# Kernel tuning notes

Measured on AMD Instinct MI355X. Metric: run time of the kernel, lower is better.

The kernel has to match this reference:

```python
import jax, jax.numpy as jnp
import numpy as np

NUM_HEADS = 16


def spike(x):
    # forward of SpikeFunction: Heaviside step
    return (x > 0).astype(x.dtype)


def setup_inputs() -> dict:
    key = jax.random.key(0)
    ks = jax.random.split(key, 11)
    B, S, D = 2, 2048, 1024
    s = 1.0 / np.sqrt(D)
    return {
        "query": jax.random.normal(ks[0], (B, S, D), jnp.float32),
        "key": jax.random.normal(ks[1], (B, S, D), jnp.float32),
        "value": jax.random.normal(ks[2], (B, S, D), jnp.float32),
        "Wq": jax.random.normal(ks[3], (D, D), jnp.float32) * s,
        "bq": jnp.zeros((D,), jnp.float32),
        "Wk": jax.random.normal(ks[4], (D, D), jnp.float32) * s,
        "bk": jnp.zeros((D,), jnp.float32),
        "Wv": jax.random.normal(ks[5], (D, D), jnp.float32) * s,
        "bv": jnp.zeros((D,), jnp.float32),
        "Wo": jax.random.normal(ks[6], (D, D), jnp.float32) * s,
        "bo": jnp.zeros((D,), jnp.float32),
    }


def reference(query, key, value, Wq, bq, Wk, bk, Wv, bv, Wo, bo):
    B, S, D = query.shape
    H = NUM_HEADS
    hd = D // H
    # torch Linear: x @ W.T + b
    q = (query @ Wq.T + bq).reshape(B, S, H, hd).transpose(0, 2, 1, 3)
    k = (key @ Wk.T + bk).reshape(B, S, H, hd).transpose(0, 2, 1, 3)
    v = (value @ Wv.T + bv).reshape(B, S, H, hd).transpose(0, 2, 1, 3)
    scale = 1.0 / np.sqrt(hd).astype(np.float32)
    scores = jnp.einsum('bhqd,bhkd->bhqk', q, k) * scale  # [B,H,S,S]
    attn = spike(scores)  # elementwise threshold instead of softmax
    ctx = jnp.einsum('bhqk,bhkd->bhqd', attn, v)
    ctx = ctx.transpose(0, 2, 1, 3).reshape(B, S, D)
    out = ctx @ Wo.T + bo
    return out, attn
```

## Files before the change

kernel.cpp:

```cpp
#include <hip/hip_runtime.h>


#define SEQ 2048
#define DIM 1024
#define NH 16
#define HD 64
#define BATCH 2
#define MROWS (BATCH * SEQ)
#define BHT (BATCH * NH)

typedef __attribute__((ext_vector_type(8))) short short8;
typedef __attribute__((ext_vector_type(4))) float f4;
typedef unsigned short ushort;

__device__ __forceinline__ f4 mfma16(short8 a, short8 b, f4 c) {
    return __builtin_amdgcn_mfma_f32_16x16x32_bf16(a, b, c, 0, 0, 0);
}
__device__ __forceinline__ ushort rne16(float x) {
    union { float f; unsigned u; } a; a.f = x;
    return (ushort)((a.u + 0x7fffu + ((a.u >> 16) & 1u)) >> 16);
}
__device__ __forceinline__ void split2(float x, ushort& h, ushort& l) {
    union { float f; unsigned u; } a; a.f = x;
    unsigned hu = a.u & 0xffff0000u;
    h = (ushort)(hu >> 16);
    union { unsigned u; float f; } hb; hb.u = hu;
    l = rne16(x - hb.f);
}
__device__ __forceinline__ short8 ld8(const ushort* p) { return *(const short8*)p; }

__global__ __launch_bounds__(256) void wconv(const float* __restrict__ Wq,
                                             const float* __restrict__ Wk,
                                             const float* __restrict__ Wv,
                                             const float* __restrict__ Wo,
                                             ushort* __restrict__ Wqh, ushort* __restrict__ Wql,
                                             ushort* __restrict__ Wkh, ushort* __restrict__ Wkl,
                                             ushort* __restrict__ Wvb, ushort* __restrict__ Wob) {
    int i = (blockIdx.x * 256 + threadIdx.x) * 4;
    int job = blockIdx.y;
    const float* src = job == 0 ? Wq : job == 1 ? Wk : job == 2 ? Wv : Wo;
    float4 w = *(const float4*)&src[i];
    float xs[4] = {w.x, w.y, w.z, w.w};
    if (job < 2) {
        ushort h[4], l[4];
#pragma unroll
        for (int j = 0; j < 4; ++j) split2(xs[j], h[j], l[j]);
        ushort* ph = job ? Wkh : Wqh;
        ushort* pl = job ? Wkl : Wql;
        *(short4*)&ph[i] = make_short4(h[0], h[1], h[2], h[3]);
        *(short4*)&pl[i] = make_short4(l[0], l[1], l[2], l[3]);
    } else {
        ushort* po = job == 2 ? Wvb : Wob;
        *(short4*)&po[i] = make_short4(rne16(xs[0]), rne16(xs[1]), rne16(xs[2]), rne16(xs[3]));
    }
}

template <int B>
__device__ __forceinline__ void ld_qk(const float* __restrict__ X, const ushort* __restrict__ Wh,
                                      const ushort* __restrict__ Wl, int m0, int n0, int la, int qd,
                                      int k0, float4 (&xA)[2][2][2], short8 (&wH)[2][4],
                                      short8 (&wL)[2][4]) {
#pragma unroll
    for (int ms = 0; ms < 2; ++ms) {
        const float* ap = &X[(size_t)(m0 + ms * 16 + la) * DIM + k0 + qd * 8];
        xA[B][ms][0] = *(const float4*)ap;
        xA[B][ms][1] = *(const float4*)(ap + 4);
    }
#pragma unroll
    for (int ns = 0; ns < 4; ++ns) {
        size_t wi = (size_t)(n0 + ns * 16 + la) * DIM + k0 + qd * 8;
        wH[B][ns] = ld8(&Wh[wi]);
        wL[B][ns] = ld8(&Wl[wi]);
    }
}

template <int B>
__device__ __forceinline__ void fma_qk(float4 (&xA)[2][2][2], short8 (&wH)[2][4],
                                       short8 (&wL)[2][4], f4 (&acc)[2][4]) {
    short8 ahi[2], alo[2];
#pragma unroll
    for (int ms = 0; ms < 2; ++ms) {
        float xs[8] = {xA[B][ms][0].x, xA[B][ms][0].y, xA[B][ms][0].z, xA[B][ms][0].w,
                       xA[B][ms][1].x, xA[B][ms][1].y, xA[B][ms][1].z, xA[B][ms][1].w};
#pragma unroll
        for (int j = 0; j < 8; ++j) {
            ushort h, l;
            split2(xs[j], h, l);
            ahi[ms][j] = (short)h;
            alo[ms][j] = (short)l;
        }
    }
#pragma unroll
    for (int ns = 0; ns < 4; ++ns)
#pragma unroll
        for (int ms = 0; ms < 2; ++ms) {
            acc[ms][ns] = mfma16(alo[ms], wH[B][ns], acc[ms][ns]);
            acc[ms][ns] = mfma16(ahi[ms], wL[B][ns], acc[ms][ns]);
            acc[ms][ns] = mfma16(ahi[ms], wH[B][ns], acc[ms][ns]);
        }
}

template <int B>
__device__ __forceinline__ void ld_v(const float* __restrict__ X, const ushort* __restrict__ Wb,
                                     int m0, int n0, int la, int qd, int k0,
                                     float4 (&xA)[2][2][2], short8 (&wH)[2][4]) {
#pragma unroll
    for (int ms = 0; ms < 2; ++ms) {
        const float* ap = &X[(size_t)(m0 + ms * 16 + la) * DIM + k0 + qd * 8];
        xA[B][ms][0] = *(const float4*)ap;
        xA[B][ms][1] = *(const float4*)(ap + 4);
    }
#pragma unroll
    for (int ns = 0; ns < 4; ++ns)
        wH[B][ns] = ld8(&Wb[(size_t)(n0 + ns * 16 + la) * DIM + k0 + qd * 8]);
}

template <int B>
__device__ __forceinline__ void fma_v(float4 (&xA)[2][2][2], short8 (&wH)[2][4], f4 (&acc)[2][4]) {
    short8 a[2];
#pragma unroll
    for (int ms = 0; ms < 2; ++ms) {
        float xs[8] = {xA[B][ms][0].x, xA[B][ms][0].y, xA[B][ms][0].z, xA[B][ms][0].w,
                       xA[B][ms][1].x, xA[B][ms][1].y, xA[B][ms][1].z, xA[B][ms][1].w};
#pragma unroll
        for (int j = 0; j < 8; ++j) a[ms][j] = (short)rne16(xs[j]);
    }
#pragma unroll
    for (int ns = 0; ns < 4; ++ns)
#pragma unroll
        for (int ms = 0; ms < 2; ++ms) acc[ms][ns] = mfma16(a[ms], wH[B][ns], acc[ms][ns]);
}

__global__ __launch_bounds__(256, 2) void proj_qkv(
    const float* __restrict__ query, const float* __restrict__ key, const float* __restrict__ value,
    const ushort* __restrict__ Wqh, const ushort* __restrict__ Wql,
    const ushort* __restrict__ Wkh, const ushort* __restrict__ Wkl,
    const ushort* __restrict__ Wvb,
    const float* __restrict__ bq, const float* __restrict__ bk, const float* __restrict__ bv,
    ushort* __restrict__ Qhi, ushort* __restrict__ Qlo,
    ushort* __restrict__ Khi, ushort* __restrict__ Klo, ushort* __restrict__ Vt) {
    const int z = blockIdx.z;
    const int t = threadIdx.x, wave = t >> 6, lane = t & 63;
    const int la = lane & 15, qd = lane >> 4;
    const int m0 = blockIdx.x * 128 + wave * 32;
    const int n0 = blockIdx.y * 64;

    float4 xA[2][2][2];
    short8 wH[2][4], wL[2][4];
    f4 acc[2][4] = {};

    if (z < 2) {
        const float* X = z ? key : query;
        const ushort* Wh = z ? Wkh : Wqh;
        const ushort* Wl = z ? Wkl : Wql;
        ld_qk<0>(X, Wh, Wl, m0, n0, la, qd, 0, xA, wH, wL);
        for (int k0 = 0; k0 < DIM; k0 += 64) {
            ld_qk<1>(X, Wh, Wl, m0, n0, la, qd, k0 + 32, xA, wH, wL);
            fma_qk<0>(xA, wH, wL, acc);
            ld_qk<0>(X, Wh, Wl, m0, n0, la, qd, (k0 + 64) & (DIM - 1), xA, wH, wL);
            fma_qk<1>(xA, wH, wL, acc);
        }
        const float* bias = z ? bk : bq;
        ushort* Oh = z ? Khi : Qhi;
        ushort* Ol = z ? Klo : Qlo;
#pragma unroll
        for (int ns = 0; ns < 4; ++ns) {
            int n = n0 + ns * 16 + la;
            float bvv = bias[n];
            int h = n >> 6, d = n & 63;
#pragma unroll
            for (int ms = 0; ms < 2; ++ms)
#pragma unroll
                for (int r = 0; r < 4; ++r) {
                    int m = m0 + ms * 16 + qd * 4 + r;
                    int b = m >> 11, s = m & 2047;
                    ushort hh, ll;
                    split2(acc[ms][ns][r] + bvv, hh, ll);
                    size_t o = ((size_t)(b * NH + h) * SEQ + s) * HD + d;
                    Oh[o] = hh;
                    Ol[o] = ll;
                }
        }
    } else {
        __shared__ ushort Ts[4][64][40];
        ld_v<0>(value, Wvb, m0, n0, la, qd, 0, xA, wH);
        for (int k0 = 0; k0 < DIM; k0 += 64) {
            ld_v<1>(value, Wvb, m0, n0, la, qd, k0 + 32, xA, wH);
            fma_v<0>(xA, wH, acc);
            ld_v<0>(value, Wvb, m0, n0, la, qd, (k0 + 64) & (DIM - 1), xA, wH);
            fma_v<1>(xA, wH, acc);
        }
#pragma unroll
        for (int ns = 0; ns < 4; ++ns) {
            float bvv = bv[n0 + ns * 16 + la];
#pragma unroll
            for (int ms = 0; ms < 2; ++ms)
#pragma unroll
                for (int r = 0; r < 4; ++r)
                    Ts[wave][ns * 16 + la][ms * 16 + qd * 4 + r] = rne16(acc[ms][ns][r] + bvv);
        }
        int b = m0 >> 11, s0 = m0 & 2047, h = n0 >> 6;
        size_t vbase = (size_t)(b * NH + h) * HD * SEQ;
#pragma unroll
        for (int it = 0; it < 4; ++it) {
            int d = it * 16 + (lane >> 2), sc = (lane & 3) * 8;
            short8 v0 = *(const short8*)&Ts[wave][d][sc];
            *(short8*)&Vt[vbase + (size_t)d * SEQ + s0 + sc] = v0;
        }
    }
}

template <int B>
__device__ __forceinline__ void ld_at(const ushort* __restrict__ Khi, const ushort* __restrict__ Klo,
                                      const ushort* __restrict__ Vt, int bh, int c0, int la, int qd,
                                      short8 (&kH)[2][2][2], short8 (&kL)[2][2][2],
                                      short8 (&vB)[2][4]) {
#pragma unroll
    for (int n2 = 0; n2 < 2; ++n2)
#pragma unroll
        for (int ks = 0; ks < 2; ++ks) {
            size_t ki = ((size_t)bh * SEQ + c0 + n2 * 16 + la) * HD + ks * 32 + qd * 8;
            kH[B][n2][ks] = ld8(&Khi[ki]);
            kL[B][n2][ks] = ld8(&Klo[ki]);
        }
#pragma unroll
    for (int ns = 0; ns < 4; ++ns)
        vB[B][ns] = ld8(&Vt[((size_t)bh * HD + ns * 16 + la) * SEQ + c0 + qd * 8]);
}

template <int B>
__device__ __forceinline__ void half_at(ushort (*Ps)[40], float* __restrict__ attn,
                                        int bh, int q0, int c0, int wave, int lane, int la, int qd,
                                        short8 (&qhi)[2][2], short8 (&qlo)[2][2],
                                        short8 (&kH)[2][2][2], short8 (&kL)[2][2][2],
                                        short8 (&vB)[2][4], f4 (&cacc)[2][4]) {
    f4 s[2][2] = {};
#pragma unroll
    for (int n2 = 0; n2 < 2; ++n2)
#pragma unroll
        for (int ks = 0; ks < 2; ++ks)
#pragma unroll
            for (int ms = 0; ms < 2; ++ms) {
                s[ms][n2] = mfma16(qlo[ms][ks], kH[B][n2][ks], s[ms][n2]);
                s[ms][n2] = mfma16(qhi[ms][ks], kL[B][n2][ks], s[ms][n2]);
                s[ms][n2] = mfma16(qhi[ms][ks], kH[B][n2][ks], s[ms][n2]);
            }
#pragma unroll
    for (int ms = 0; ms < 2; ++ms)
#pragma unroll
        for (int n2 = 0; n2 < 2; ++n2)
#pragma unroll
            for (int r = 0; r < 4; ++r)
                Ps[wave * 32 + ms * 16 + qd * 4 + r][n2 * 16 + la] =
                    s[ms][n2][r] > 0.f ? (ushort)0x3f80 : (ushort)0;
#pragma unroll
    for (int it = 0; it < 4; ++it) {
        int row = it * 8 + (lane >> 3);
        short4 p = *(const short4*)&Ps[wave * 32 + row][(lane & 7) * 4];
        float4 o;
        o.x = __uint_as_float(((unsigned)(ushort)p.x) << 16);
        o.y = __uint_as_float(((unsigned)(ushort)p.y) << 16);
        o.z = __uint_as_float(((unsigned)(ushort)p.z) << 16);
        o.w = __uint_as_float(((unsigned)(ushort)p.w) << 16);
        *(float4*)&attn[((size_t)bh * SEQ + q0 + row) * SEQ + c0 + (lane & 7) * 4] = o;
    }
    short8 pa[2];
#pragma unroll
    for (int ms = 0; ms < 2; ++ms)
        pa[ms] = *(const short8*)&Ps[wave * 32 + ms * 16 + la][qd * 8];
#pragma unroll
    for (int ns = 0; ns < 4; ++ns)
#pragma unroll
        for (int ms = 0; ms < 2; ++ms) cacc[ms][ns] = mfma16(pa[ms], vB[B][ns], cacc[ms][ns]);
}

__global__ __launch_bounds__(256, 2) void attn_mfma(
    const ushort* __restrict__ Qhi, const ushort* __restrict__ Qlo,
    const ushort* __restrict__ Khi, const ushort* __restrict__ Klo,
    const ushort* __restrict__ Vt, float* __restrict__ attn, ushort* __restrict__ ctxb) {
    __shared__ ushort Ps[128][40];
    const int t = threadIdx.x, wave = t >> 6, lane = t & 63;
    const int la = lane & 15, qd = lane >> 4;
    const int bh = blockIdx.x;
    const int q0 = blockIdx.y * 128 + wave * 32;

    short8 qhi[2][2], qlo[2][2];
#pragma unroll
    for (int ms = 0; ms < 2; ++ms)
#pragma unroll
        for (int ks = 0; ks < 2; ++ks) {
            size_t qi = ((size_t)bh * SEQ + q0 + ms * 16 + la) * HD + ks * 32 + qd * 8;
            qhi[ms][ks] = ld8(&Qhi[qi]);
            qlo[ms][ks] = ld8(&Qlo[qi]);
        }

    short8 kH[2][2][2], kL[2][2][2], vB[2][4];
    f4 cacc[2][4] = {};
    ld_at<0>(Khi, Klo, Vt, bh, 0, la, qd, kH, kL, vB);
    for (int h = 0; h < 64; h += 2) {
        ld_at<1>(Khi, Klo, Vt, bh, (h + 1) * 32, la, qd, kH, kL, vB);
        half_at<0>(Ps, attn, bh, q0, h * 32, wave, lane, la, qd, qhi, qlo, kH, kL, vB, cacc);
        ld_at<0>(Khi, Klo, Vt, bh, ((h + 2) & 63) * 32, la, qd, kH, kL, vB);
        half_at<1>(Ps, attn, bh, q0, (h + 1) * 32, wave, lane, la, qd, qhi, qlo, kH, kL, vB, cacc);
    }
#pragma unroll
    for (int ns = 0; ns < 4; ++ns)
#pragma unroll
        for (int ms = 0; ms < 2; ++ms)
#pragma unroll
            for (int r = 0; r < 4; ++r) {
                int qrow = q0 + ms * 16 + qd * 4 + r;
                ctxb[((size_t)bh * SEQ + qrow) * HD + ns * 16 + la] = rne16(cacc[ms][ns][r]);
            }
}

template <int B>
__device__ __forceinline__ void ld_o(const ushort* __restrict__ Ctx, const ushort* __restrict__ Wb,
                                     int m0, int n0, int la, int qd, int k0,
                                     short8 (&aO)[2][2], short8 (&wO)[2][4]) {
#pragma unroll
    for (int ms = 0; ms < 2; ++ms) {
        int m = m0 + ms * 16 + la;
        int b = m >> 11, s = m & 2047;
        int k = k0 + qd * 8;
        int h = k >> 6, d = k & 63;
        aO[B][ms] = ld8(&Ctx[((size_t)(b * NH + h) * SEQ + s) * HD + d]);
    }
#pragma unroll
    for (int ns = 0; ns < 4; ++ns)
        wO[B][ns] = ld8(&Wb[(size_t)(n0 + ns * 16 + la) * DIM + k0 + qd * 8]);
}

__global__ __launch_bounds__(256, 2) void proj_out(const ushort* __restrict__ Ctx,
                                                   const ushort* __restrict__ Wb,
                                                   const float* __restrict__ bias,
                                                   float* __restrict__ out) {
    const int t = threadIdx.x, wave = t >> 6, lane = t & 63;
    const int la = lane & 15, qd = lane >> 4;
    const int m0 = blockIdx.x * 128 + wave * 32;
    const int n0 = blockIdx.y * 64;

    short8 aO[2][2], wO[2][4];
    f4 acc[2][4] = {};
    ld_o<0>(Ctx, Wb, m0, n0, la, qd, 0, aO, wO);
    for (int k0 = 0; k0 < DIM; k0 += 64) {
        ld_o<1>(Ctx, Wb, m0, n0, la, qd, k0 + 32, aO, wO);
#pragma unroll
        for (int ns = 0; ns < 4; ++ns)
#pragma unroll
            for (int ms = 0; ms < 2; ++ms) acc[ms][ns] = mfma16(aO[0][ms], wO[0][ns], acc[ms][ns]);
        ld_o<0>(Ctx, Wb, m0, n0, la, qd, (k0 + 64) & (DIM - 1), aO, wO);
#pragma unroll
        for (int ns = 0; ns < 4; ++ns)
#pragma unroll
            for (int ms = 0; ms < 2; ++ms) acc[ms][ns] = mfma16(aO[1][ms], wO[1][ns], acc[ms][ns]);
    }
#pragma unroll
    for (int ns = 0; ns < 4; ++ns) {
        int n = n0 + ns * 16 + la;
        float bvv = bias[n];
#pragma unroll
        for (int ms = 0; ms < 2; ++ms)
#pragma unroll
            for (int r = 0; r < 4; ++r) {
                int m = m0 + ms * 16 + qd * 4 + r;
                out[(size_t)m * DIM + n] = acc[ms][ns][r] + bvv;
            }
    }
}

extern "C" void kernel_launch(void* const* d_in, const int* in_sizes, int n_in,
                              void* d_out, int out_size, void* d_ws, size_t ws_size,
                              hipStream_t stream) {
    const float* query = (const float*)d_in[0];
    const float* key   = (const float*)d_in[1];
    const float* value = (const float*)d_in[2];
    const float* Wq = (const float*)d_in[3];
    const float* bq = (const float*)d_in[4];
    const float* Wk = (const float*)d_in[5];
    const float* bk = (const float*)d_in[6];
    const float* Wv = (const float*)d_in[7];
    const float* bv = (const float*)d_in[8];
    const float* Wo = (const float*)d_in[9];
    const float* bo = (const float*)d_in[10];

    float* out  = (float*)d_out;
    float* attn = out + (size_t)MROWS * DIM;

    const size_t NE = (size_t)MROWS * DIM;
    const size_t WE = (size_t)DIM * DIM;
    ushort* Qhi = (ushort*)d_ws;
    ushort* Qlo = Qhi + NE;
    ushort* Khi = Qlo + NE;
    ushort* Klo = Khi + NE;
    ushort* Vt  = Klo + NE;
    ushort* Wqh = Vt + NE;
    ushort* Wql = Wqh + WE;
    ushort* Wkh = Wql + WE;
    ushort* Wkl = Wkh + WE;
    ushort* Wvb = Wkl + WE;
    ushort* Wob = Wvb + WE;
    ushort* Ctx = Wqh;

    dim3 blk(256);
    hipLaunchKernelGGL(wconv, dim3(WE / 1024, 4), blk, 0, stream,
                       Wq, Wk, Wv, Wo, Wqh, Wql, Wkh, Wkl, Wvb, Wob);
    hipLaunchKernelGGL(proj_qkv, dim3(32, 16, 3), blk, 0, stream,
                       query, key, value, Wqh, Wql, Wkh, Wkl, Wvb, bq, bk, bv,
                       Qhi, Qlo, Khi, Klo, Vt);
    hipLaunchKernelGGL(attn_mfma, dim3(32, 16), blk, 0, stream,
                       Qhi, Qlo, Khi, Klo, Vt, attn, Ctx);
    hipLaunchKernelGGL(proj_out, dim3(32, 16), blk, 0, stream, Ctx, Wob, bo, out);
}
```

Baseline: 1.041 ms.

## Use nontemporal stores, direct attn writes, and MFMA priority hints in attention

Switches all global output stores (Q/K hi-lo splits, transposed V, attention map, context, final output) to nontemporal stores so they bypass cache retention. The attention map is now written straight from MFMA registers as scalar floats instead of being re-read from LDS and written as float4, which removes LDS reads but makes the stores narrower and less coalesced. It also raises wave priority around the MFMA sections with s_setprio. Intermediates such as Qhi, Khi, Vt and ctxb are read again by later kernels, so nontemporal stores on them may hurt those reads.

```diff
diff --git a/kernel.cpp b/kernel.cpp
--- a/kernel.cpp
+++ b/kernel.cpp
@@ -177,8 +177,8 @@
                     ushort hh, ll;
                     split2(acc[ms][ns][r] + bvv, hh, ll);
                     size_t o = ((size_t)(b * NH + h) * SEQ + s) * HD + d;
-                    Oh[o] = hh;
-                    Ol[o] = ll;
+                    __builtin_nontemporal_store(hh, &Oh[o]);
+                    __builtin_nontemporal_store(ll, &Ol[o]);
                 }
         }
     } else {
@@ -205,7 +205,7 @@
         for (int it = 0; it < 4; ++it) {
             int d = it * 16 + (lane >> 2), sc = (lane & 3) * 8;
             short8 v0 = *(const short8*)&Ts[wave][d][sc];
-            *(short8*)&Vt[vbase + (size_t)d * SEQ + s0 + sc] = v0;
+            __builtin_nontemporal_store(v0, (short8*)&Vt[vbase + (size_t)d * SEQ + s0 + sc]);
         }
     }
 }
@@ -230,11 +230,12 @@
 
 template <int B>
 __device__ __forceinline__ void half_at(ushort (*Ps)[40], float* __restrict__ attn,
-                                        int bh, int q0, int c0, int wave, int lane, int la, int qd,
+                                        int bh, int q0, int c0, int wave, int la, int qd,
                                         short8 (&qhi)[2][2], short8 (&qlo)[2][2],
                                         short8 (&kH)[2][2][2], short8 (&kL)[2][2][2],
                                         short8 (&vB)[2][4], f4 (&cacc)[2][4]) {
     f4 s[2][2] = {};
+    __builtin_amdgcn_s_setprio(1);
 #pragma unroll
     for (int n2 = 0; n2 < 2; ++n2)
 #pragma unroll
@@ -245,6 +246,7 @@
                 s[ms][n2] = mfma16(qhi[ms][ks], kL[B][n2][ks], s[ms][n2]);
                 s[ms][n2] = mfma16(qhi[ms][ks], kH[B][n2][ks], s[ms][n2]);
             }
+    __builtin_amdgcn_s_setprio(0);
 #pragma unroll
     for (int ms = 0; ms < 2; ++ms)
 #pragma unroll
@@ -254,24 +256,26 @@
                 Ps[wave * 32 + ms * 16 + qd * 4 + r][n2 * 16 + la] =
                     s[ms][n2][r] > 0.f ? (ushort)0x3f80 : (ushort)0;
 #pragma unroll
-    for (int it = 0; it < 4; ++it) {
-        int row = it * 8 + (lane >> 3);
-        short4 p = *(const short4*)&Ps[wave * 32 + row][(lane & 7) * 4];
-        float4 o;
-        o.x = __uint_as_float(((unsigned)(ushort)p.x) << 16);
-        o.y = __uint_as_float(((unsigned)(ushort)p.y) << 16);
-        o.z = __uint_as_float(((unsigned)(ushort)p.z) << 16);
-        o.w = __uint_as_float(((unsigned)(ushort)p.w) << 16);
-        *(float4*)&attn[((size_t)bh * SEQ + q0 + row) * SEQ + c0 + (lane & 7) * 4] = o;
-    }
+    for (int ms = 0; ms < 2; ++ms)
+#pragma unroll
+        for (int n2 = 0; n2 < 2; ++n2)
+#pragma unroll
+            for (int r = 0; r < 4; ++r) {
+                int row = ms * 16 + qd * 4 + r;
+                __builtin_nontemporal_store(
+                    s[ms][n2][r] > 0.f ? 1.0f : 0.0f,
+                    &attn[((size_t)bh * SEQ + q0 + row) * SEQ + c0 + n2 * 16 + la]);
+            }
     short8 pa[2];
 #pragma unroll
     for (int ms = 0; ms < 2; ++ms)
         pa[ms] = *(const short8*)&Ps[wave * 32 + ms * 16 + la][qd * 8];
+    __builtin_amdgcn_s_setprio(1);
 #pragma unroll
     for (int ns = 0; ns < 4; ++ns)
 #pragma unroll
         for (int ms = 0; ms < 2; ++ms) cacc[ms][ns] = mfma16(pa[ms], vB[B][ns], cacc[ms][ns]);
+    __builtin_amdgcn_s_setprio(0);
 }
 
 __global__ __launch_bounds__(256, 2) void attn_mfma(
@@ -299,9 +303,9 @@
     ld_at<0>(Khi, Klo, Vt, bh, 0, la, qd, kH, kL, vB);
     for (int h = 0; h < 64; h += 2) {
         ld_at<1>(Khi, Klo, Vt, bh, (h + 1) * 32, la, qd, kH, kL, vB);
-        half_at<0>(Ps, attn, bh, q0, h * 32, wave, lane, la, qd, qhi, qlo, kH, kL, vB, cacc);
+        half_at<0>(Ps, attn, bh, q0, h * 32, wave, la, qd, qhi, qlo, kH, kL, vB, cacc);
         ld_at<0>(Khi, Klo, Vt, bh, ((h + 2) & 63) * 32, la, qd, kH, kL, vB);
-        half_at<1>(Ps, attn, bh, q0, (h + 1) * 32, wave, lane, la, qd, qhi, qlo, kH, kL, vB, cacc);
+        half_at<1>(Ps, attn, bh, q0, (h + 1) * 32, wave, la, qd, qhi, qlo, kH, kL, vB, cacc);
     }
 #pragma unroll
     for (int ns = 0; ns < 4; ++ns)
@@ -310,7 +314,9 @@
 #pragma unroll
             for (int r = 0; r < 4; ++r) {
                 int qrow = q0 + ms * 16 + qd * 4 + r;
-                ctxb[((size_t)bh * SEQ + qrow) * HD + ns * 16 + la] = rne16(cacc[ms][ns][r]);
+                __builtin_nontemporal_store(
+                    rne16(cacc[ms][ns][r]),
+                    &ctxb[((size_t)bh * SEQ + qrow) * HD + ns * 16 + la]);
             }
 }
 
@@ -364,7 +370,7 @@
 #pragma unroll
             for (int r = 0; r < 4; ++r) {
                 int m = m0 + ms * 16 + qd * 4 + r;
-                out[(size_t)m * DIM + n] = acc[ms][ns][r] + bvv;
+                __builtin_nontemporal_store(acc[ms][ns][r] + bvv, &out[(size_t)m * DIM + n]);
             }
     }
 }
```

Measured after the change: 1.175 ms. 1.13x slower.
